# Kernel optimization log

Measured on AMD Instinct MI355X. Metric: run time of the kernel, lower is better.

The kernel has to match this reference:

```python
import jax, jax.numpy as jnp
import numpy as np

HIP_L, HIP_R = 11, 12          # hip joint indices along V
K_LIST = (2, 3, 4, 5)          # soft-selector kNN MoE k values
TAU = 0.35                     # tau_center for ball softmax
EPS = 1e-6


def _sym_norm(A):
    # D^{-1/2} A D^{-1/2} without materializing diag matrices
    d = A.sum(-1)
    dis = jax.lax.rsqrt(d + EPS)
    return dis[..., :, None] * A * dis[..., None, :]


def _knn_adj(pos, k):
    # pos: (N, M, 3) -> 0/1 kNN adjacency (+I self loop, diag ends up 2 as in torch ref)
    M = pos.shape[1]
    diff = pos[:, :, None, :] - pos[:, None, :, :]
    d = jnp.sqrt(jnp.sum(diff * diff, axis=-1))  # (N, M, M) euclidean cdist
    idx = jax.lax.top_k(-d, k)[1]                # (N, M, k) k smallest distances (incl. self)
    A = jax.nn.one_hot(idx, M, dtype=pos.dtype).sum(2)  # scatter 1.0 at kNN columns
    return A + jnp.eye(M, dtype=pos.dtype)


def setup_inputs() -> dict:
    key = jax.random.key(0)
    k1, k2 = jax.random.split(key)
    N, C, T, V, M = 64, 8, 300, 17, 12
    x = jax.random.normal(k1, (N, C, T, V, M), jnp.float32)
    alpha_logits = jax.random.normal(k2, (len(K_LIST),), jnp.float32) * 0.1
    lambda_fuse = jnp.array([0.1], jnp.float32)
    tag_gate = jnp.array([1.0], jnp.float32)
    return {"x": x, "alpha_logits": alpha_logits,
            "lambda_fuse": lambda_fuse, "tag_gate": tag_gate}


def reference(x, alpha_logits, lambda_fuse, tag_gate):
    N, C, T, V, M = x.shape
    # hip-root position averaged over time: (N, M, 3)
    root3 = 0.5 * (x[:, 0:3, :, HIP_L, :] + x[:, 0:3, :, HIP_R, :])  # (N,3,T,M)
    pos = root3.mean(2).transpose(0, 2, 1)                           # (N,M,3)

    # kNN mixture-of-graphs, sym-normalized, detached (detach_adj=True)
    A_knn_stack = jnp.stack([_sym_norm(_knn_adj(pos, k)) for k in K_LIST], 1)  # (N,K,M,M)
    A_knn_stack = jax.lax.stop_gradient(A_knn_stack)
    alpha = jax.nn.softmax(alpha_logits)          # global selector, temp=1
    A_knn = jnp.einsum('k,nkij->nij', alpha, A_knn_stack)

    # soft ball-star graph
    s = x[:, 3].mean((1, 2))                      # (N,M) ball score
    p = jax.nn.softmax(s / TAU, axis=1)
    A_ball = p[:, :, None] + p[:, None, :] + jnp.eye(M, dtype=x.dtype)
    A_ball = jax.lax.stop_gradient(_sym_norm(A_ball))

    # adaptive ball weight from confidence of p (NOT detached)
    w = jnp.clip((jnp.max(p, 1, keepdims=True) - 1.0 / M) / (1.0 - 1.0 / M + EPS), 0.0, 1.0)
    A = w[:, :, None] * A_ball + (1.0 - w[:, :, None]) * A_knn  # (N,M,M)

    # message passing across persons on hip-root features, fused back residually
    root = 0.5 * (x[:, :, :, HIP_L, :] + x[:, :, :, HIP_R, :])  # (N,C,T,M)
    agg = jnp.einsum('nuv,nctv->nctu', A, root)                 # (N,C,T,M)
    g = jnp.tanh(tag_gate[0])  # ramp=1 (ramp_epochs=0), gate_max=1
    return x + g * lambda_fuse[0] * (agg - root)[:, :, :, None, :]
```

## Files before the change

### kernel.cpp

```cpp
#include <hip/hip_runtime.h>
#include <math.h>

#define N_ 64
#define C_ 8
#define T_ 300
#define V_ 17
#define M_ 12
#define EPSF 1e-6f
#define TAUF 0.35f

typedef float f32x4 __attribute__((ext_vector_type(4)));


#define TSPLIT 10
#define TCH (T_ / TSPLIT)

__global__ __launch_bounds__(256) void k_reduce(const float* __restrict__ x,
                                                float* __restrict__ ws_part) {
    const int n = blockIdx.x;
    const int by = blockIdx.y;
    const int t0 = by * TCH;
    const int tid = threadIdx.x;
    __shared__ float pos_acc[36];
    __shared__ float s_acc[12];
    if (tid < 36) pos_acc[tid] = 0.f;
    if (tid < 12) s_acc[tid] = 0.f;
    __syncthreads();

    {
        const f32x4* xs4 = (const f32x4*)(x + ((size_t)(n * C_ + 3) * T_ + t0) * 204);
        f32x4 a0 = {0.f, 0.f, 0.f, 0.f}, a1 = a0, a2 = a0;
        #pragma unroll
        for (int k = 0; k < 6; ++k) {
            int f = tid + 256 * k;
            if (f < TCH * 51) {
                f32x4 v = xs4[f];
                if (k % 3 == 0) a0 += v;
                else if (k % 3 == 1) a1 += v;
                else a2 += v;
            }
        }
        int mb0 = (4 * tid) % 12;
        int mb1 = (4 * (tid + 1)) % 12;
        int mb2 = (4 * (tid + 2)) % 12;
        #pragma unroll
        for (int c = 0; c < 4; ++c) {
            atomicAdd(&s_acc[mb0 + c], a0[c]);
            atomicAdd(&s_acc[mb1 + c], a1[c]);
            atomicAdd(&s_acc[mb2 + c], a2[c]);
        }
    }

    for (int e = tid; e < 3 * TCH * 6; e += 256) {
        int d = e / (TCH * 6);
        int rem = e % (TCH * 6);
        int tt = rem / 6, q = rem % 6;
        const f32x4* xp4 = (const f32x4*)(x + ((size_t)(n * C_ + d) * T_ + t0 + tt) * 204 + 132);
        f32x4 v = xp4[q];
        int m0 = (q % 3) * 4;
        atomicAdd(&pos_acc[d * 12 + m0 + 0], v.x);
        atomicAdd(&pos_acc[d * 12 + m0 + 1], v.y);
        atomicAdd(&pos_acc[d * 12 + m0 + 2], v.z);
        atomicAdd(&pos_acc[d * 12 + m0 + 3], v.w);
    }
    __syncthreads();

    float* slot = ws_part + (size_t)(n * TSPLIT + by) * 48;
    if (tid < 36) slot[tid] = pos_acc[tid];
    if (tid < 12) slot[36 + tid] = s_acc[tid];
}

__global__ __launch_bounds__(64) void k_adj(const float* __restrict__ ws_part,
                                            const float* __restrict__ alpha_logits,
                                            float* __restrict__ ws_A) {
    const int n = blockIdx.x;
    const int tid = threadIdx.x;
    __shared__ float raw[48];
    __shared__ float posx[12], posy[12], posz[12];
    __shared__ float dist[144];
    __shared__ int ord[60];
    __shared__ float p_s[12];
    __shared__ float alpha_s[4];
    __shared__ float w_s;

    if (tid < 48) {
        float a = 0.f;
        #pragma unroll
        for (int j = 0; j < TSPLIT; ++j) a += ws_part[(size_t)(n * TSPLIT + j) * 48 + tid];
        raw[tid] = a;
    }
    __syncthreads();

    const float PSC = 0.5f / (float)T_;
    if (tid < 12) {
        posx[tid] = raw[0 * 12 + tid] * PSC;
        posy[tid] = raw[1 * 12 + tid] * PSC;
        posz[tid] = raw[2 * 12 + tid] * PSC;
    }
    if (tid == 0) {
        float l0 = alpha_logits[0], l1 = alpha_logits[1], l2 = alpha_logits[2], l3 = alpha_logits[3];
        float mx = fmaxf(fmaxf(l0, l1), fmaxf(l2, l3));
        float e0 = expf(l0 - mx), e1 = expf(l1 - mx), e2 = expf(l2 - mx), e3 = expf(l3 - mx);
        float s = e0 + e1 + e2 + e3;
        alpha_s[0] = e0 / s; alpha_s[1] = e1 / s; alpha_s[2] = e2 / s; alpha_s[3] = e3 / s;
    }
    if (tid == 1) {
        const float SSC = 1.f / ((float)(T_ * V_) * TAUF);
        float sv[12];
        float mx = -1e30f;
        #pragma unroll
        for (int m = 0; m < 12; ++m) { sv[m] = raw[36 + m] * SSC; mx = fmaxf(mx, sv[m]); }
        float sum = 0.f;
        #pragma unroll
        for (int m = 0; m < 12; ++m) { sv[m] = expf(sv[m] - mx); sum += sv[m]; }
        float maxp = 0.f;
        #pragma unroll
        for (int m = 0; m < 12; ++m) { sv[m] = sv[m] / sum; p_s[m] = sv[m]; maxp = fmaxf(maxp, sv[m]); }
        float w = (maxp - 1.f / 12.f) / (1.f - 1.f / 12.f + EPSF);
        w_s = fminf(fmaxf(w, 0.f), 1.f);
    }
    __syncthreads();

    for (int e = tid; e < 144; e += 64) {
        int i = e / 12, j = e % 12;
        float dx = posx[i] - posx[j], dy = posy[i] - posy[j], dz = posz[i] - posz[j];
        dist[e] = sqrtf(dx * dx + dy * dy + dz * dz);
    }
    __syncthreads();

    if (tid < 12) {
        int i = tid, mask = 0;
        #pragma unroll
        for (int r = 0; r < 5; ++r) {
            float bd = 1e30f; int bj = -1;
            #pragma unroll
            for (int j = 0; j < 12; ++j) {
                if (!((mask >> j) & 1)) {
                    float dd = dist[i * 12 + j];
                    if (dd < bd) { bd = dd; bj = j; }
                }
            }
            ord[i * 5 + r] = bj; mask |= (1 << bj);
        }
    }
    __syncthreads();

    float w = w_s;
    for (int e = tid; e < 144; e += 64) {
        int i = e / 12, j = e % 12;
        int rank = 5;
        #pragma unroll
        for (int r = 4; r >= 0; --r) if (ord[i * 5 + r] == j) rank = r;
        float diag = (i == j) ? 1.f : 0.f;
        float aknn = 0.f;
        #pragma unroll
        for (int kk = 0; kk < 4; ++kk) {
            int K = kk + 2;
            float val = ((rank < K) ? 1.f : 0.f) + diag;
            aknn += alpha_s[kk] * val / ((float)(K + 1) + EPSF);
        }
        float pi = p_s[i], pj = p_s[j];
        float di = 12.f * pi + 2.f, dj = 12.f * pj + 2.f;
        float ab = (pi + pj + diag) * rsqrtf(di + EPSF) * rsqrtf(dj + EPSF);
        ws_A[n * 144 + e] = w * ab + (1.f - w) * aknn;
    }
}

#define RT 30
__global__ __launch_bounds__(256) void k_main(const float* __restrict__ x,
                                              const float* __restrict__ ws_A,
                                              const float* __restrict__ lambda_fuse,
                                              const float* __restrict__ tag_gate,
                                              float* __restrict__ out) {
    const int n = blockIdx.y;
    const int r0 = blockIdx.x * RT;
    const int tid = threadIdx.x;
    __shared__ f32x4 xs4[RT * 51];
    __shared__ float Ash[144];
    __shared__ float delta_sh[RT * 12];
    float* xs = (float*)xs4;

    if (tid < 36) ((f32x4*)Ash)[tid] = ((const f32x4*)(ws_A + n * 144))[tid];
    float scale = tanhf(tag_gate[0]) * lambda_fuse[0];

    const float* xn = x + (size_t)n * 2400 * 204;
    float* on = out + (size_t)n * 2400 * 204;
    const f32x4* x4 = (const f32x4*)(xn + (size_t)r0 * 204);
    f32x4* o4 = (f32x4*)(on + (size_t)r0 * 204);

    for (int f = tid; f < RT * 51; f += 256) xs4[f] = x4[f];
    __syncthreads();

    for (int e = tid; e < RT * 12; e += 256) {
        int r = e / 12, u = e % 12;
        const float* row = xs + r * 204;
        float acc = 0.f;
        #pragma unroll
        for (int v = 0; v < 12; ++v) {
            float rv = 0.5f * (row[132 + v] + row[144 + v]);
            acc += Ash[u * 12 + v] * rv;
        }
        float ru = 0.5f * (row[132 + u] + row[144 + u]);
        delta_sh[e] = scale * (acc - ru);
    }
    __syncthreads();

    for (int f = tid; f < RT * 51; f += 256) {
        int r = f / 51, j = f % 51;
        int m0 = (4 * j) % 12;
        f32x4 v = xs4[f];
        const float* d = &delta_sh[r * 12 + m0];
        v.x += d[0]; v.y += d[1]; v.z += d[2]; v.w += d[3];
        __builtin_nontemporal_store(v, &o4[f]);
    }
}

extern "C" void kernel_launch(void* const* d_in, const int* in_sizes, int n_in,
                              void* d_out, int out_size, void* d_ws, size_t ws_size,
                              hipStream_t stream) {
    const float* x = (const float*)d_in[0];
    const float* alpha_logits = (const float*)d_in[1];
    const float* lambda_fuse = (const float*)d_in[2];
    const float* tag_gate = (const float*)d_in[3];
    float* out = (float*)d_out;

    float* ws = (float*)d_ws;
    float* ws_part = ws;
    float* ws_A = ws + 64 * TSPLIT * 48;

    k_reduce<<<dim3(N_, TSPLIT), dim3(256), 0, stream>>>(x, ws_part);
    k_adj<<<dim3(N_), dim3(64), 0, stream>>>(ws_part, alpha_logits, ws_A);
    k_main<<<dim3(2400 / RT, N_), dim3(256), 0, stream>>>(x, ws_A, lambda_fuse, tag_gate, out);
}
```

Baseline: 254.8 us.

## Fuse adjacency construction into main kernel and double time split of reduction

The separate per-sample adjacency kernel is removed; each main-kernel block now recomputes the 12x12 mixed adjacency in shared memory from the partial sums while its x tile loads, which drops one launch and its serialization gap. The reduction kernel's time split goes from 10 to 20 chunks, so each block does half the loads and the grid gets more parallelism. In exchange, every one of the 80 blocks per sample repeats the small top-k and softmax work and reads 20 partial slots.

```diff
diff --git a/kernel.cpp b/kernel.cpp
--- a/kernel.cpp
+++ b/kernel.cpp
@@ -12,7 +12,7 @@
 typedef float f32x4 __attribute__((ext_vector_type(4)));
 
 
-#define TSPLIT 10
+#define TSPLIT 20
 #define TCH (T_ / TSPLIT)
 
 __global__ __launch_bounds__(256) void k_reduce(const float* __restrict__ x,
@@ -31,12 +31,12 @@
         const f32x4* xs4 = (const f32x4*)(x + ((size_t)(n * C_ + 3) * T_ + t0) * 204);
         f32x4 a0 = {0.f, 0.f, 0.f, 0.f}, a1 = a0, a2 = a0;
         #pragma unroll
-        for (int k = 0; k < 6; ++k) {
+        for (int k = 0; k < 3; ++k) {
             int f = tid + 256 * k;
             if (f < TCH * 51) {
                 f32x4 v = xs4[f];
-                if (k % 3 == 0) a0 += v;
-                else if (k % 3 == 1) a1 += v;
+                if (k == 0) a0 += v;
+                else if (k == 1) a1 += v;
                 else a2 += v;
             }
         }
@@ -70,11 +70,19 @@
     if (tid < 12) slot[36 + tid] = s_acc[tid];
 }
 
-__global__ __launch_bounds__(64) void k_adj(const float* __restrict__ ws_part,
-                                            const float* __restrict__ alpha_logits,
-                                            float* __restrict__ ws_A) {
-    const int n = blockIdx.x;
+#define RT 30
+__global__ __launch_bounds__(256) void k_main(const float* __restrict__ x,
+                                              const float* __restrict__ ws_part,
+                                              const float* __restrict__ alpha_logits,
+                                              const float* __restrict__ lambda_fuse,
+                                              const float* __restrict__ tag_gate,
+                                              float* __restrict__ out) {
+    const int n = blockIdx.y;
+    const int r0 = blockIdx.x * RT;
     const int tid = threadIdx.x;
+    __shared__ f32x4 xs4[RT * 51];
+    __shared__ float Ash[144];
+    __shared__ float delta_sh[RT * 12];
     __shared__ float raw[48];
     __shared__ float posx[12], posy[12], posz[12];
     __shared__ float dist[144];
@@ -82,6 +90,14 @@
     __shared__ float p_s[12];
     __shared__ float alpha_s[4];
     __shared__ float w_s;
+    float* xs = (float*)xs4;
+
+    const float* xn = x + (size_t)n * 2400 * 204;
+    float* on = out + (size_t)n * 2400 * 204;
+    const f32x4* x4 = (const f32x4*)(xn + (size_t)r0 * 204);
+    f32x4* o4 = (f32x4*)(on + (size_t)r0 * 204);
+
+    for (int f = tid; f < RT * 51; f += 256) xs4[f] = x4[f];
 
     if (tid < 48) {
         float a = 0.f;
@@ -89,6 +105,7 @@
         for (int j = 0; j < TSPLIT; ++j) a += ws_part[(size_t)(n * TSPLIT + j) * 48 + tid];
         raw[tid] = a;
     }
+    float scale = tanhf(tag_gate[0]) * lambda_fuse[0];
     __syncthreads();
 
     const float PSC = 0.5f / (float)T_;
@@ -104,7 +121,7 @@
         float s = e0 + e1 + e2 + e3;
         alpha_s[0] = e0 / s; alpha_s[1] = e1 / s; alpha_s[2] = e2 / s; alpha_s[3] = e3 / s;
     }
-    if (tid == 1) {
+    if (tid == 64) {
         const float SSC = 1.f / ((float)(T_ * V_) * TAUF);
         float sv[12];
         float mx = -1e30f;
@@ -121,10 +138,10 @@
     }
     __syncthreads();
 
-    for (int e = tid; e < 144; e += 64) {
-        int i = e / 12, j = e % 12;
+    if (tid < 144) {
+        int i = tid / 12, j = tid % 12;
         float dx = posx[i] - posx[j], dy = posy[i] - posy[j], dz = posz[i] - posz[j];
-        dist[e] = sqrtf(dx * dx + dy * dy + dz * dz);
+        dist[tid] = sqrtf(dx * dx + dy * dy + dz * dz);
     }
     __syncthreads();
 
@@ -145,9 +162,8 @@
     }
     __syncthreads();
 
-    float w = w_s;
-    for (int e = tid; e < 144; e += 64) {
-        int i = e / 12, j = e % 12;
+    if (tid < 144) {
+        int i = tid / 12, j = tid % 12;
         int rank = 5;
         #pragma unroll
         for (int r = 4; r >= 0; --r) if (ord[i * 5 + r] == j) rank = r;
@@ -162,33 +178,9 @@
         float pi = p_s[i], pj = p_s[j];
         float di = 12.f * pi + 2.f, dj = 12.f * pj + 2.f;
         float ab = (pi + pj + diag) * rsqrtf(di + EPSF) * rsqrtf(dj + EPSF);
-        ws_A[n * 144 + e] = w * ab + (1.f - w) * aknn;
-    }
-}
-
-#define RT 30
-__global__ __launch_bounds__(256) void k_main(const float* __restrict__ x,
-                                              const float* __restrict__ ws_A,
-                                              const float* __restrict__ lambda_fuse,
-                                              const float* __restrict__ tag_gate,
-                                              float* __restrict__ out) {
-    const int n = blockIdx.y;
-    const int r0 = blockIdx.x * RT;
-    const int tid = threadIdx.x;
-    __shared__ f32x4 xs4[RT * 51];
-    __shared__ float Ash[144];
-    __shared__ float delta_sh[RT * 12];
-    float* xs = (float*)xs4;
-
-    if (tid < 36) ((f32x4*)Ash)[tid] = ((const f32x4*)(ws_A + n * 144))[tid];
-    float scale = tanhf(tag_gate[0]) * lambda_fuse[0];
-
-    const float* xn = x + (size_t)n * 2400 * 204;
-    float* on = out + (size_t)n * 2400 * 204;
-    const f32x4* x4 = (const f32x4*)(xn + (size_t)r0 * 204);
-    f32x4* o4 = (f32x4*)(on + (size_t)r0 * 204);
-
-    for (int f = tid; f < RT * 51; f += 256) xs4[f] = x4[f];
+        float w = w_s;
+        Ash[tid] = w * ab + (1.f - w) * aknn;
+    }
     __syncthreads();
 
     for (int e = tid; e < RT * 12; e += 256) {
@@ -224,11 +216,9 @@
     const float* tag_gate = (const float*)d_in[3];
     float* out = (float*)d_out;
 
-    float* ws = (float*)d_ws;
-    float* ws_part = ws;
-    float* ws_A = ws + 64 * TSPLIT * 48;
+    float* ws_part = (float*)d_ws;
 
     k_reduce<<<dim3(N_, TSPLIT), dim3(256), 0, stream>>>(x, ws_part);
-    k_adj<<<dim3(N_), dim3(64), 0, stream>>>(ws_part, alpha_logits, ws_A);
-    k_main<<<dim3(2400 / RT, N_), dim3(256), 0, stream>>>(x, ws_A, lambda_fuse, tag_gate, out);
+    k_main<<<dim3(2400 / RT, N_), dim3(256), 0, stream>>>(x, ws_part, alpha_logits,
+                                                          lambda_fuse, tag_gate, out);
 }
```

After: 256.2 us. About the same (+0.6%).
